# Kernel tuning notes

Hardware: AMD Instinct MI355X
Metric: run time of the kernel (lower is better)

Reference implementation:

```python
import jax, jax.numpy as jnp
import numpy as np

B, C, H, W = 8, 2048, 14, 14
NUM_CLASSES, WORD_DIM, INTER_DIM = 80, 300, 1024


def setup_inputs() -> dict:
    key = jax.random.key(0)
    ks = jax.random.split(key, 8)
    s = 0.02
    return {
        "image_features": jax.random.normal(ks[0], (B, C, H, W), jnp.float32),
        "word_features": jax.random.normal(ks[1], (NUM_CLASSES, WORD_DIM), jnp.float32),
        "W1": jax.random.normal(ks[2], (INTER_DIM, C), jnp.float32) * s,
        "W2": jax.random.normal(ks[3], (INTER_DIM, WORD_DIM), jnp.float32) * s,
        "W3": jax.random.normal(ks[4], (INTER_DIM, INTER_DIM), jnp.float32) * s,
        "b3": jax.random.normal(ks[5], (INTER_DIM,), jnp.float32) * s,
        "Wa": jax.random.normal(ks[6], (1, INTER_DIM), jnp.float32) * s,
        "ba": jax.random.normal(ks[7], (1,), jnp.float32) * s,
        "num_classes": NUM_CLASSES,
    }


def reference(image_features, word_features, W1, W2, W3, b3, Wa, ba, num_classes):
    b, c, h, w = image_features.shape
    # [s, b, c] with s = h*w (spatial locations)
    img = image_features.reshape(b, c, h * w).transpose(2, 0, 1)
    f_wh = img @ W1.T                      # [s, b, D]
    f_wd = word_features @ W2.T            # [n, D]
    # additive-attention score MLP; broadcast to [s, b, n, D]
    lb = jnp.tanh(f_wh[:, :, None, :] * f_wd[None, None, :, :]) @ W3.T + b3
    coef = (lb @ Wa.T + ba)[..., 0]        # [s, b, n]
    coef = jax.nn.softmax(coef, axis=0)    # softmax over spatial locations
    # weighted sum over spatial dim -> [b, n, c]
    return jnp.einsum('sbc,sbn->bnc', img, coef)
```

## Files before the change

### kernel.cpp

```cpp
#include <hip/hip_runtime.h>
#include <math.h>

#define SB 196
#define SP 224
#define NB 8
#define NC 2048
#define ND 1024
#define NN 80
#define NW 300
#define CH 16
#define DCH (ND / CH)
#define NT 4
#define NJ (NB * SB)
#define NJP 1600
#define PITCH 40

typedef __bf16 v8bf __attribute__((ext_vector_type(8)));
typedef __bf16 v4bf __attribute__((ext_vector_type(4)));
typedef float  f32x4 __attribute__((ext_vector_type(4)));

__global__ __launch_bounds__(256) void kcast_x(const float* __restrict__ X,
                                               const float* __restrict__ W1,
                                               const float* __restrict__ W3,
                                               const float* __restrict__ Wa,
                                               __bf16* __restrict__ Xt,
                                               __bf16* __restrict__ Xhi,
                                               __bf16* __restrict__ Xlo,
                                               __bf16* __restrict__ W1b,
                                               float* __restrict__ vpart) {
    const int t = threadIdx.x;
    if (blockIdx.z == 9) {
        if (blockIdx.x < 16) {
            const int e0 = blockIdx.x * 64;
            const int d  = blockIdx.y * 256 + t;
            float p = 0.f;
            #pragma unroll 8
            for (int e = e0; e < e0 + 64; ++e)
                p += Wa[e] * W3[(size_t)e * ND + d];
            vpart[blockIdx.x * ND + d] = p;
        } else if (blockIdx.x == 16) {
            const int tid = blockIdx.y * 256 + t;
            uint4 z = make_uint4(0u, 0u, 0u, 0u);
            uint4* p = (uint4*)(Xt + (size_t)NJ * NC);
            #pragma unroll
            for (int r = 0; r < 8; ++r) p[tid + r * 1024] = z;
        }
        return;
    }
    if (blockIdx.z == 8) {
        unsigned int slice_tid = (blockIdx.x * 4 + blockIdx.y) * 256 + t;
        #pragma unroll 4
        for (int r = 0; r < 16; ++r) {
            size_t i = ((size_t)slice_tid + (size_t)r * 32768) * 4;
            float4 f = *(const float4*)(W1 + i);
            v4bf o;
            o[0] = (__bf16)f.x; o[1] = (__bf16)f.y;
            o[2] = (__bf16)f.z; o[3] = (__bf16)f.w;
            *(v4bf*)(W1b + i) = o;
        }
        return;
    }
    __shared__ float tile[64][65];
    const int b  = blockIdx.z;
    const int c0 = blockIdx.x * 64;
    const int s0 = blockIdx.y * 64;
    const float* Xb = X + (size_t)b * NC * SB;
    {
        int ss = t & 63, cbase = t >> 6;
        #pragma unroll
        for (int r = 0; r < 16; ++r) {
            int cc = cbase + 4 * r;
            float val = (s0 + ss < SB) ? Xb[(size_t)(c0 + cc) * SB + s0 + ss] : 0.f;
            tile[cc][ss] = val;
        }
    }
    __syncthreads();
    {
        int cc = t & 63, sbase = t >> 6;
        #pragma unroll
        for (int r = 0; r < 16; ++r) {
            int ss = sbase + 4 * r;
            if (s0 + ss < SB)
                Xt[((size_t)b * SB + s0 + ss) * NC + c0 + cc] = (__bf16)tile[cc][ss];
        }
    }
    {
        int ss = t & 63, cbase = t >> 6;
        int sg = s0 + ss;
        #pragma unroll
        for (int r = 0; r < 16; ++r) {
            int cc = cbase + 4 * r;
            if (sg < SP) {
                float val = (sg < SB) ? tile[cc][ss] : 0.f;
                __bf16 h = (__bf16)val;
                __bf16 l = (__bf16)(val - (float)h);
                size_t base = ((size_t)b * NC + c0 + cc) * SP + sg;
                Xhi[base] = h;
                Xlo[base] = l;
            }
        }
    }
}

__global__ __launch_bounds__(256) void k1_mfma(const __bf16* __restrict__ Xt,
                                               const __bf16* __restrict__ W1b,
                                               float* __restrict__ F,
                                               const float* __restrict__ word,
                                               const float* __restrict__ W2,
                                               const float* __restrict__ vpart,
                                               float2* __restrict__ wpack) {
    const int t = threadIdx.x;
    if (blockIdx.y >= 25) {
        __shared__ __align__(16) float lword[NW];
        const int e = (blockIdx.y - 25) * 16 + blockIdx.x;
        const int n = e >> 2;
        const int d = (e & 3) * 256 + t;
        for (int i = t; i < NW; i += 256) lword[i] = word[(size_t)n * NW + i];
        __syncthreads();
        const float4* wr = (const float4*)(W2 + (size_t)d * NW);
        const float4* l4 = (const float4*)lword;
        float acc = 0.f;
        #pragma unroll 5
        for (int i = 0; i < NW / 4; ++i) {
            float4 a = wr[i], b = l4[i];
            acc += a.x * b.x + a.y * b.y + a.z * b.z + a.w * b.w;
        }
        float vv = 0.f;
        #pragma unroll
        for (int p = 0; p < 16; ++p) vv += vpart[p * ND + d];
        float2 o;
        o.x = 2.8853900817779268f * acc;
        o.y = -2.f * vv;
        wpack[(size_t)n * ND + d] = o;
        return;
    }
    __shared__ __align__(16) __bf16 lA[64 * PITCH];
    __shared__ __align__(16) __bf16 lB[64 * PITCH];
    const int d0   = blockIdx.x * 64;
    const int j0   = blockIdx.y * 64;
    const int lane = t & 63;
    const int wave = t >> 6;
    const int doff = (wave & 1) * 32;
    const int joff = (wave >> 1) * 32;
    const int quad = lane >> 4;
    const int l16  = lane & 15;

    f32x4 acc[2][2] = {};

    const int rr = t >> 2;
    const int cc = (t & 3) * 8;
    const __bf16* Ag = W1b + (size_t)(d0 + rr) * NC + cc;
    const __bf16* Bg = Xt + (size_t)(j0 + rr) * NC + cc;
    __bf16* lAw = lA + rr * PITCH + cc;
    __bf16* lBw = lB + rr * PITCH + cc;

    const __bf16* rA0 = lA + (doff + l16) * PITCH + quad * 8;
    const __bf16* rA1 = rA0 + 16 * PITCH;
    const __bf16* rB0 = lB + (joff + l16) * PITCH + quad * 8;
    const __bf16* rB1 = rB0 + 16 * PITCH;

    for (int k0 = 0; k0 < NC; k0 += 32) {
        uint4 a  = *(const uint4*)(Ag + k0);
        uint4 bv = *(const uint4*)(Bg + k0);
        __syncthreads();
        *(uint4*)lAw = a;
        *(uint4*)lBw = bv;
        __syncthreads();
        v8bf a0 = *(const v8bf*)rA0;
        v8bf a1 = *(const v8bf*)rA1;
        v8bf b0 = *(const v8bf*)rB0;
        v8bf b1 = *(const v8bf*)rB1;
        acc[0][0] = __builtin_amdgcn_mfma_f32_16x16x32_bf16(a0, b0, acc[0][0], 0, 0, 0);
        acc[0][1] = __builtin_amdgcn_mfma_f32_16x16x32_bf16(a0, b1, acc[0][1], 0, 0, 0);
        acc[1][0] = __builtin_amdgcn_mfma_f32_16x16x32_bf16(a1, b0, acc[1][0], 0, 0, 0);
        acc[1][1] = __builtin_amdgcn_mfma_f32_16x16x32_bf16(a1, b1, acc[1][1], 0, 0, 0);
    }
    #pragma unroll
    for (int i = 0; i < 2; ++i) {
        #pragma unroll
        for (int jj = 0; jj < 2; ++jj) {
            int j = j0 + joff + jj * 16 + l16;
            if (j < NJ) {
                int b = j / SB;
                int s = j - b * SB;
                float* Fp = F + ((size_t)b * ND + d0 + doff + i * 16 + quad * 4) * SB + s;
                #pragma unroll
                for (int r = 0; r < 4; ++r)
                    Fp[(size_t)r * SB] = acc[i][jj][r];
            }
        }
    }
}

__global__ __launch_bounds__(256) void k2a(const float* __restrict__ F,
                                           const float2* __restrict__ wpack,
                                           float* __restrict__ part) {
    const int n0  = blockIdx.x * NT;
    const int ch  = blockIdx.z;
    const int idx = blockIdx.y * 256 + threadIdx.x;
    const bool valid = idx < (NB * SB);
    const int iv = valid ? idx : 0;
    const int b  = iv / SB;
    const int s  = iv - b * SB;
    const float*  Fp  = F + ((size_t)b * ND + ch * DCH) * SB + s;
    const float4* wp0 = (const float4*)(wpack + (size_t)(n0 + 0) * ND + ch * DCH);
    const float4* wp1 = (const float4*)(wpack + (size_t)(n0 + 1) * ND + ch * DCH);
    const float4* wp2 = (const float4*)(wpack + (size_t)(n0 + 2) * ND + ch * DCH);
    const float4* wp3 = (const float4*)(wpack + (size_t)(n0 + 3) * ND + ch * DCH);
    float a0 = 0.f, a1 = 0.f, a2 = 0.f, a3 = 0.f;
    #pragma unroll 4
    for (int d2 = 0; d2 < DCH / 2; ++d2) {
        float f0 = Fp[(size_t)(2 * d2)     * SB];
        float f1 = Fp[(size_t)(2 * d2 + 1) * SB];
        float4 w0 = wp0[d2];
        float4 w1 = wp1[d2];
        float4 w2 = wp2[d2];
        float4 w3 = wp3[d2];
        float e00 = __builtin_amdgcn_exp2f(f0 * w0.x);
        float e01 = __builtin_amdgcn_exp2f(f1 * w0.z);
        float e10 = __builtin_amdgcn_exp2f(f0 * w1.x);
        float e11 = __builtin_amdgcn_exp2f(f1 * w1.z);
        float e20 = __builtin_amdgcn_exp2f(f0 * w2.x);
        float e21 = __builtin_amdgcn_exp2f(f1 * w2.z);
        float e30 = __builtin_amdgcn_exp2f(f0 * w3.x);
        float e31 = __builtin_amdgcn_exp2f(f1 * w3.z);
        a0 = fmaf(w0.y, __builtin_amdgcn_rcpf(1.f + e00), a0);
        a0 = fmaf(w0.w, __builtin_amdgcn_rcpf(1.f + e01), a0);
        a1 = fmaf(w1.y, __builtin_amdgcn_rcpf(1.f + e10), a1);
        a1 = fmaf(w1.w, __builtin_amdgcn_rcpf(1.f + e11), a1);
        a2 = fmaf(w2.y, __builtin_amdgcn_rcpf(1.f + e20), a2);
        a2 = fmaf(w2.w, __builtin_amdgcn_rcpf(1.f + e21), a2);
        a3 = fmaf(w3.y, __builtin_amdgcn_rcpf(1.f + e30), a3);
        a3 = fmaf(w3.w, __builtin_amdgcn_rcpf(1.f + e31), a3);
    }
    if (valid) {
        size_t base = ((size_t)ch * NB + b) * NN;
        part[(base + n0 + 0) * 256 + s] = a0;
        part[(base + n0 + 1) * 256 + s] = a1;
        part[(base + n0 + 2) * 256 + s] = a2;
        part[(base + n0 + 3) * 256 + s] = a3;
    }
}

__global__ __launch_bounds__(256) void k2b(const float* __restrict__ part,
                                           __bf16* __restrict__ coefh,
                                           __bf16* __restrict__ coefl) {
    __shared__ float red[256];
    const int n = blockIdx.x;
    const int b = blockIdx.y;
    const int t = threadIdx.x;
    float acc = 0.f;
    #pragma unroll
    for (int ch = 0; ch < CH; ++ch)
        acc += part[(((size_t)ch * NB + b) * NN + n) * 256 + t];

    red[t] = (t < SB) ? acc : -1e30f;
    __syncthreads();
    #pragma unroll
    for (int off = 128; off > 0; off >>= 1) {
        if (t < off) red[t] = fmaxf(red[t], red[t + off]);
        __syncthreads();
    }
    float m = red[0];
    __syncthreads();
    float p = (t < SB) ? __expf(acc - m) : 0.f;
    red[t] = p;
    __syncthreads();
    #pragma unroll
    for (int off = 128; off > 0; off >>= 1) {
        if (t < off) red[t] += red[t + off];
        __syncthreads();
    }
    float inv = 1.f / red[0];
    if (t < SP) {
        float val = (t < SB) ? p * inv : 0.f;
        __bf16 h = (__bf16)val;
        __bf16 l = (__bf16)(val - (float)h);
        size_t base = ((size_t)b * NN + n) * SP + t;
        coefh[base] = h;
        coefl[base] = l;
    }
}

__global__ __launch_bounds__(256) void k3_mfma(const __bf16* __restrict__ Xhi,
                                               const __bf16* __restrict__ Xlo,
                                               const __bf16* __restrict__ coefh,
                                               const __bf16* __restrict__ coefl,
                                               float* __restrict__ out) {
    const int t     = threadIdx.x;
    const int wave  = t >> 6;
    const int lane  = t & 63;
    const int quad  = lane >> 4;
    const int l16   = lane & 15;
    const int b     = blockIdx.y;
    const int cbase = blockIdx.x * 64 + wave * 16;

    const __bf16* Bh = Xhi + ((size_t)b * NC + cbase + l16) * SP + quad * 8;
    const __bf16* Bl = Xlo + ((size_t)b * NC + cbase + l16) * SP + quad * 8;
    const __bf16* Ah = coefh + ((size_t)b * NN + l16) * SP + quad * 8;
    const __bf16* Al = coefl + ((size_t)b * NN + l16) * SP + quad * 8;

    f32x4 acc[5] = {};

    #pragma unroll
    for (int k0 = 0; k0 < SP; k0 += 32) {
        v8bf bh = *(const v8bf*)(Bh + k0);
        v8bf bl = *(const v8bf*)(Bl + k0);
        #pragma unroll
        for (int mt = 0; mt < 5; ++mt) {
            v8bf ah = *(const v8bf*)(Ah + (size_t)mt * 16 * SP + k0);
            v8bf al = *(const v8bf*)(Al + (size_t)mt * 16 * SP + k0);
            acc[mt] = __builtin_amdgcn_mfma_f32_16x16x32_bf16(ah, bh, acc[mt], 0, 0, 0);
            acc[mt] = __builtin_amdgcn_mfma_f32_16x16x32_bf16(al, bh, acc[mt], 0, 0, 0);
            acc[mt] = __builtin_amdgcn_mfma_f32_16x16x32_bf16(ah, bl, acc[mt], 0, 0, 0);
        }
    }
    #pragma unroll
    for (int mt = 0; mt < 5; ++mt) {
        #pragma unroll
        for (int r = 0; r < 4; ++r) {
            int n = mt * 16 + quad * 4 + r;
            out[((size_t)b * NN + n) * NC + cbase + l16] = acc[mt][r];
        }
    }
}

extern "C" void kernel_launch(void* const* d_in, const int* in_sizes, int n_in,
                              void* d_out, int out_size, void* d_ws, size_t ws_size,
                              hipStream_t stream) {
    const float* X    = (const float*)d_in[0];
    const float* word = (const float*)d_in[1];
    const float* W1   = (const float*)d_in[2];
    const float* W2   = (const float*)d_in[3];
    const float* W3   = (const float*)d_in[4];
    const float* Wa   = (const float*)d_in[6];
    float* out = (float*)d_out;

    char* ws = (char*)d_ws;
    float*  vpart = (float*)ws;
    float2* wpack = (float2*)(vpart + 16 * ND);
    float*  part  = (float*)(wpack + (size_t)NN * ND);
    __bf16* coefh = (__bf16*)(part + (size_t)CH * NB * NN * 256);
    __bf16* coefl = coefh + (size_t)NB * NN * SP;
    __bf16* W1b   = coefl + (size_t)NB * NN * SP;
    __bf16* Xt    = W1b + (size_t)ND * NC;
    float*  F     = (float*)(Xt + (size_t)NJP * NC);
    __bf16* Xhi   = (__bf16*)(F + (size_t)NB * ND * SB);
    __bf16* Xlo   = Xhi + (size_t)NB * NC * SP;

    kcast_x<<<dim3(32, 4, 10),    256, 0, stream>>>(X, W1, W3, Wa, Xt, Xhi, Xlo, W1b, vpart);
    k1_mfma<<<dim3(16, 45),       256, 0, stream>>>(Xt, W1b, F, word, W2, vpart, wpack);
    k2a    <<<dim3(NN / NT, 7, CH), 256, 0, stream>>>(F, wpack, part);
    k2b    <<<dim3(NN, NB),       256, 0, stream>>>(part, coefh, coefl);
    k3_mfma<<<dim3(NC / 64, NB),  256, 0, stream>>>(Xhi, Xlo, coefh, coefl, out);
}
```

Before: 165.3 us.

## Split K dimension of k1 GEMM across two thread halves with LDS reduction

Raises the k1_mfma block size to 512 threads. Each 256-thread half computes the 64x64 tile over half of the K=2048 reduction using its own LDS buffers, and the two partial sums are then combined through shared memory before the store. This halves the serial K loop per wave and doubles the waves per block, aiming at more latency hiding in the GEMM that builds F. The cost is an extra LDS reduction step, two more barriers, and half of the threads sitting idle in the word-projection blocks.

```diff
diff --git a/kernel.cpp b/kernel.cpp
--- a/kernel.cpp
+++ b/kernel.cpp
@@ -102,7 +102,7 @@
     }
 }
 
-__global__ __launch_bounds__(256) void k1_mfma(const __bf16* __restrict__ Xt,
+__global__ __launch_bounds__(512) void k1_mfma(const __bf16* __restrict__ Xt,
                                                const __bf16* __restrict__ W1b,
                                                float* __restrict__ F,
                                                const float* __restrict__ word,
@@ -114,43 +114,53 @@
         __shared__ __align__(16) float lword[NW];
         const int e = (blockIdx.y - 25) * 16 + blockIdx.x;
         const int n = e >> 2;
-        const int d = (e & 3) * 256 + t;
-        for (int i = t; i < NW; i += 256) lword[i] = word[(size_t)n * NW + i];
-        __syncthreads();
-        const float4* wr = (const float4*)(W2 + (size_t)d * NW);
-        const float4* l4 = (const float4*)lword;
-        float acc = 0.f;
-        #pragma unroll 5
-        for (int i = 0; i < NW / 4; ++i) {
-            float4 a = wr[i], b = l4[i];
-            acc += a.x * b.x + a.y * b.y + a.z * b.z + a.w * b.w;
-        }
-        float vv = 0.f;
-        #pragma unroll
-        for (int p = 0; p < 16; ++p) vv += vpart[p * ND + d];
-        float2 o;
-        o.x = 2.8853900817779268f * acc;
-        o.y = -2.f * vv;
-        wpack[(size_t)n * ND + d] = o;
+        if (t < 256) {
+            for (int i = t; i < NW; i += 256) lword[i] = word[(size_t)n * NW + i];
+        }
+        __syncthreads();
+        if (t < 256) {
+            const int d = (e & 3) * 256 + t;
+            const float4* wr = (const float4*)(W2 + (size_t)d * NW);
+            const float4* l4 = (const float4*)lword;
+            float acc = 0.f;
+            #pragma unroll 5
+            for (int i = 0; i < NW / 4; ++i) {
+                float4 a = wr[i], b = l4[i];
+                acc += a.x * b.x + a.y * b.y + a.z * b.z + a.w * b.w;
+            }
+            float vv = 0.f;
+            #pragma unroll
+            for (int p = 0; p < 16; ++p) vv += vpart[p * ND + d];
+            float2 o;
+            o.x = 2.8853900817779268f * acc;
+            o.y = -2.f * vv;
+            wpack[(size_t)n * ND + d] = o;
+        }
         return;
     }
-    __shared__ __align__(16) __bf16 lA[64 * PITCH];
-    __shared__ __align__(16) __bf16 lB[64 * PITCH];
+    __shared__ __align__(16) char smem[4 * 64 * PITCH * 2];
+    const int half = t >> 8;
+    const int tt   = t & 255;
+    __bf16* lA = (__bf16*)smem + half * 64 * PITCH;
+    __bf16* lB = (__bf16*)smem + 2 * 64 * PITCH + half * 64 * PITCH;
+    float*  red = (float*)smem;
+
     const int d0   = blockIdx.x * 64;
     const int j0   = blockIdx.y * 64;
-    const int lane = t & 63;
-    const int wave = t >> 6;
-    const int doff = (wave & 1) * 32;
-    const int joff = (wave >> 1) * 32;
+    const int lane = tt & 63;
+    const int w4   = tt >> 6;
+    const int doff = (w4 & 1) * 32;
+    const int joff = (w4 >> 1) * 32;
     const int quad = lane >> 4;
     const int l16  = lane & 15;
 
     f32x4 acc[2][2] = {};
 
-    const int rr = t >> 2;
-    const int cc = (t & 3) * 8;
-    const __bf16* Ag = W1b + (size_t)(d0 + rr) * NC + cc;
-    const __bf16* Bg = Xt + (size_t)(j0 + rr) * NC + cc;
+    const int rr = tt >> 2;
+    const int cc = (tt & 3) * 8;
+    const int kbase = half * (NC / 2);
+    const __bf16* Ag = W1b + (size_t)(d0 + rr) * NC + kbase + cc;
+    const __bf16* Bg = Xt + (size_t)(j0 + rr) * NC + kbase + cc;
     __bf16* lAw = lA + rr * PITCH + cc;
     __bf16* lBw = lB + rr * PITCH + cc;
 
@@ -159,7 +169,7 @@
     const __bf16* rB0 = lB + (joff + l16) * PITCH + quad * 8;
     const __bf16* rB1 = rB0 + 16 * PITCH;
 
-    for (int k0 = 0; k0 < NC; k0 += 32) {
+    for (int k0 = 0; k0 < NC / 2; k0 += 32) {
         uint4 a  = *(const uint4*)(Ag + k0);
         uint4 bv = *(const uint4*)(Bg + k0);
         __syncthreads();
@@ -175,18 +185,36 @@
         acc[1][0] = __builtin_amdgcn_mfma_f32_16x16x32_bf16(a1, b0, acc[1][0], 0, 0, 0);
         acc[1][1] = __builtin_amdgcn_mfma_f32_16x16x32_bf16(a1, b1, acc[1][1], 0, 0, 0);
     }
-    #pragma unroll
-    for (int i = 0; i < 2; ++i) {
-        #pragma unroll
-        for (int jj = 0; jj < 2; ++jj) {
-            int j = j0 + joff + jj * 16 + l16;
-            if (j < NJ) {
-                int b = j / SB;
-                int s = j - b * SB;
-                float* Fp = F + ((size_t)b * ND + d0 + doff + i * 16 + quad * 4) * SB + s;
+
+    __syncthreads();
+    if (half == 1) {
+        #pragma unroll
+        for (int i = 0; i < 2; ++i)
+            #pragma unroll
+            for (int jj = 0; jj < 2; ++jj)
                 #pragma unroll
                 for (int r = 0; r < 4; ++r)
-                    Fp[(size_t)r * SB] = acc[i][jj][r];
+                    red[(doff + i * 16 + quad * 4 + r) * 64 + (joff + jj * 16 + l16)]
+                        = acc[i][jj][r];
+    }
+    __syncthreads();
+    if (half == 0) {
+        #pragma unroll
+        for (int i = 0; i < 2; ++i) {
+            #pragma unroll
+            for (int jj = 0; jj < 2; ++jj) {
+                int j = j0 + joff + jj * 16 + l16;
+                if (j < NJ) {
+                    int b = j / SB;
+                    int s = j - b * SB;
+                    float* Fp = F + ((size_t)b * ND + d0 + doff + i * 16 + quad * 4) * SB + s;
+                    #pragma unroll
+                    for (int r = 0; r < 4; ++r) {
+                        float v = acc[i][jj][r]
+                                + red[(doff + i * 16 + quad * 4 + r) * 64 + (joff + jj * 16 + l16)];
+                        Fp[(size_t)r * SB] = v;
+                    }
+                }
             }
         }
     }
@@ -349,7 +377,7 @@
     __bf16* Xlo   = Xhi + (size_t)NB * NC * SP;
 
     kcast_x<<<dim3(32, 4, 10),    256, 0, stream>>>(X, W1, W3, Wa, Xt, Xhi, Xlo, W1b, vpart);
-    k1_mfma<<<dim3(16, 45),       256, 0, stream>>>(Xt, W1b, F, word, W2, vpart, wpack);
+    k1_mfma<<<dim3(16, 45),       512, 0, stream>>>(Xt, W1b, F, word, W2, vpart, wpack);
     k2a    <<<dim3(NN / NT, 7, CH), 256, 0, stream>>>(F, wpack, part);
     k2b    <<<dim3(NN, NB),       256, 0, stream>>>(part, coefh, coefl);
     k3_mfma<<<dim3(NC / 64, NB),  256, 0, stream>>>(Xhi, Xlo, coefh, coefl, out);
```

After: 164.8 us. About the same (-0.3%).
